# Kernel optimization log

Hardware: AMD Instinct MI355X
Metric: run time of the kernel (lower is better)

The kernel has to match this reference:

```python
import jax, jax.numpy as jnp
import numpy as np

B = 131072
IN_DIM = 21   # velocity_dim * (past_frame + 2) = 3 * 7
HID = 512
OUT_DIM = 21  # 7 waypoints * 3 coords
SEG = 0.5     # segment width in in_same_segment
WW = 0.5      # rescale weight for same-segment elements
INVALID = -10000.0
VALID_THRESH = -5000.0


def setup_inputs() -> dict:
    key = jax.random.key(0)
    ks = jax.random.split(key, 9)
    velocities = jax.random.normal(ks[0], (B, IN_DIM), dtype=jnp.float32)
    gt = jax.random.normal(ks[1], (B, 7, 3), dtype=jnp.float32)
    # emulate warp_gt padding: some trailing waypoints are invalid sentinels
    pad_mask = jax.random.bernoulli(ks[2], 0.2, (B, 7, 1))
    gt = jnp.where(pad_mask, jnp.float32(INVALID), gt)
    s1 = 1.0 / np.sqrt(IN_DIM)
    s2 = 1.0 / np.sqrt(HID)
    W1 = jax.random.uniform(ks[3], (HID, IN_DIM), jnp.float32, -s1, s1)
    b1 = jax.random.uniform(ks[4], (HID,), jnp.float32, -s1, s1)
    W2 = jax.random.uniform(ks[5], (HID, HID), jnp.float32, -s2, s2)
    b2 = jax.random.uniform(ks[6], (HID,), jnp.float32, -s2, s2)
    W3 = jax.random.uniform(ks[7], (OUT_DIM, HID), jnp.float32, -s2, s2)
    b3 = jax.random.uniform(ks[8], (OUT_DIM,), jnp.float32, -s2, s2)
    return {"velocities": velocities, "gt": gt,
            "W1": W1, "b1": b1, "W2": W2, "b2": b2, "W3": W3, "b3": b3}


def reference(velocities, gt, W1, b1, W2, b2, W3, b3):
    # plan_head MLP: 21 -> 512 -> 512 -> 21
    h = jax.nn.relu(velocities @ W1.T + b1)
    h = jax.nn.relu(h @ W2.T + b2)
    out = h @ W3.T + b3                      # [B, 21]
    pred = out.reshape(-1, 7, 3)             # waypoints x1..x7, 3 coords each
    # segment-conditional weighted L1 loss (vectorized form of the Python loop)
    valid = gt > VALID_THRESH
    same_seg = jnp.floor(pred / SEG) == jnp.floor(gt / SEG)
    w = jnp.where(valid & same_seg, jnp.float32(WW), jnp.float32(1.0))
    diff = jnp.abs(pred * w - gt * w)
    num = jnp.sum(jnp.where(valid, diff, 0.0))
    den = jnp.sum(valid.astype(jnp.float32))
    return num / den
```

## Files before the change

### kernel.cpp

```cpp
#include <hip/hip_runtime.h>
#include <hip/hip_bf16.h>

typedef __bf16 bf16_t;
typedef __bf16 bf16x4 __attribute__((ext_vector_type(4)));
typedef __bf16 bf16x8 __attribute__((ext_vector_type(8)));
typedef float f32x4 __attribute__((ext_vector_type(4)));

#define IN_DIM 21
#define HID 512
#define OUT_DIM 21
#define M_TILE 128
#define THREADS 1024

__device__ __forceinline__ int swz(int row, int col) {
    return col ^ ((row & 7) << 3);
}

__global__ void prep_kernel(const float* __restrict__ W1, const float* __restrict__ W2,
                            const float* __restrict__ W3,
                            bf16_t* __restrict__ W1f, bf16_t* __restrict__ W2f,
                            bf16_t* __restrict__ W3f, float* __restrict__ accum) {
    if (blockIdx.x == 0 && threadIdx.x == 0) {
        accum[0] = 0.0f; accum[1] = 0.0f;
        ((unsigned*)accum)[2] = 0u;
    }
    int i = blockIdx.x * blockDim.x + threadIdx.x;
    int stride = gridDim.x * blockDim.x;
    const int NW2 = HID * HID;
    const int NW1 = 32 * 512;
    const int NW3 = 16 * 2 * 512;
    for (; i < NW2 + NW1 + NW3; i += stride) {
        if (i < NW2) {
            int j = i & 7, lane = (i >> 3) & 63, ntile = (i >> 9) & 31, kstep = i >> 14;
            int n = ntile * 16 + (lane & 15);
            int k = kstep * 32 + (lane >> 4) * 8 + j;
            W2f[i] = (bf16_t)W2[n * HID + k];
        } else if (i < NW2 + NW1) {
            int t = i - NW2;
            int j = t & 7, lane = (t >> 3) & 63, ntile = t >> 9;
            int n = ntile * 16 + (lane & 15);
            int k = (lane >> 4) * 8 + j;
            W1f[t] = (k < IN_DIM) ? (bf16_t)W1[n * IN_DIM + k] : (bf16_t)0.0f;
        } else {
            int t = i - NW2 - NW1;
            int j = t & 7, lane = (t >> 3) & 63, ot = (t >> 9) & 1, kstep = t >> 10;
            int o = ot * 16 + (lane & 15);
            int k = kstep * 32 + (lane >> 4) * 8 + j;
            W3f[t] = (o < OUT_DIM) ? (bf16_t)W3[o * HID + k] : (bf16_t)0.0f;
        }
    }
}

__global__ __launch_bounds__(THREADS, 4)
void fused_kernel(const float* __restrict__ V, const float* __restrict__ gt,
                  const float* __restrict__ b1, const float* __restrict__ b2,
                  const float* __restrict__ b3,
                  const bf16_t* __restrict__ W1f, const bf16_t* __restrict__ W2f,
                  const bf16_t* __restrict__ W3f, float* __restrict__ accum,
                  float* __restrict__ out) {
    __shared__ __align__(16) bf16_t vlds[M_TILE][40];
    __shared__ __align__(16) bf16_t h[M_TILE][HID];
    __shared__ float redbuf[32];

    const int tid  = threadIdx.x;
    const int wave = tid >> 6;
    const int lane = tid & 63;
    const int quad = lane >> 4;
    const int l16  = lane & 15;
    const int mh   = wave >> 3;
    const int ng   = wave & 7;
    const int sx   = (l16 & 7) << 3;
    const long row0 = (long)blockIdx.x * M_TILE;

    const bf16_t* w2p = W2f + ng * 4 * 512 + lane * 8;
    bf16x8 awA[4], awB[4];
    #pragma unroll
    for (int nt = 0; nt < 4; ++nt)
        awA[nt] = *reinterpret_cast<const bf16x8*>(w2p + nt * 512);

    for (int idx = tid; idx < M_TILE * 32; idx += THREADS) {
        int r = idx >> 5, c = idx & 31;
        float v = (c < IN_DIM) ? V[(row0 + r) * IN_DIM + c] : 0.0f;
        vlds[r][c] = (bf16_t)v;
    }
    __syncthreads();

    {
        bf16x8 bv[4];
        #pragma unroll
        for (int mt = 0; mt < 4; ++mt)
            bv[mt] = *reinterpret_cast<const bf16x8*>(&vlds[mh * 64 + mt * 16 + l16][quad * 8]);
        #pragma unroll
        for (int nt = 0; nt < 4; ++nt) {
            int ntile = ng * 4 + nt;
            bf16x8 aw = *reinterpret_cast<const bf16x8*>(W1f + ntile * 512 + lane * 8);
            f32x4 bias = *reinterpret_cast<const f32x4*>(b1 + ntile * 16 + quad * 4);
            int n0 = ntile * 16 + quad * 4;
            #pragma unroll
            for (int mt = 0; mt < 4; ++mt) {
                f32x4 c = {0.0f, 0.0f, 0.0f, 0.0f};
                c = __builtin_amdgcn_mfma_f32_16x16x32_bf16(aw, bv[mt], c, 0, 0, 0);
                bf16x4 pk;
                #pragma unroll
                for (int r = 0; r < 4; ++r) {
                    float v = c[r] + bias[r];
                    pk[r] = (bf16_t)(v > 0.0f ? v : 0.0f);
                }
                int m = mh * 64 + mt * 16 + l16;
                *reinterpret_cast<bf16x4*>(&h[m][n0 ^ sx]) = pk;
            }
        }
    }
    __syncthreads();

    {
        f32x4 acc[4][4];
        #pragma unroll
        for (int mt = 0; mt < 4; ++mt)
            #pragma unroll
            for (int nt = 0; nt < 4; ++nt)
                acc[mt][nt] = (f32x4){0.0f, 0.0f, 0.0f, 0.0f};

        #pragma unroll 1
        for (int ks = 0; ks < 16; ks += 2) {
            #pragma unroll
            for (int nt = 0; nt < 4; ++nt)
                awB[nt] = *reinterpret_cast<const bf16x8*>(w2p + (ks + 1) * 16384 + nt * 512);
            {
                bf16x8 bh[4];
                #pragma unroll
                for (int mt = 0; mt < 4; ++mt)
                    bh[mt] = *reinterpret_cast<const bf16x8*>(
                        &h[mh * 64 + mt * 16 + l16][(ks * 32 + quad * 8) ^ sx]);
                #pragma unroll
                for (int mt = 0; mt < 4; ++mt)
                    #pragma unroll
                    for (int nt = 0; nt < 4; ++nt)
                        acc[mt][nt] = __builtin_amdgcn_mfma_f32_16x16x32_bf16(awA[nt], bh[mt], acc[mt][nt], 0, 0, 0);
            }
            #pragma unroll
            for (int nt = 0; nt < 4; ++nt)
                awA[nt] = *reinterpret_cast<const bf16x8*>(w2p + (ks + 2) * 16384 + nt * 512);
            {
                bf16x8 bh[4];
                #pragma unroll
                for (int mt = 0; mt < 4; ++mt)
                    bh[mt] = *reinterpret_cast<const bf16x8*>(
                        &h[mh * 64 + mt * 16 + l16][((ks + 1) * 32 + quad * 8) ^ sx]);
                #pragma unroll
                for (int mt = 0; mt < 4; ++mt)
                    #pragma unroll
                    for (int nt = 0; nt < 4; ++nt)
                        acc[mt][nt] = __builtin_amdgcn_mfma_f32_16x16x32_bf16(awB[nt], bh[mt], acc[mt][nt], 0, 0, 0);
            }
        }
        __syncthreads();

        #pragma unroll
        for (int nt = 0; nt < 4; ++nt) {
            int ntile = ng * 4 + nt;
            f32x4 bias = *reinterpret_cast<const f32x4*>(b2 + ntile * 16 + quad * 4);
            int n0 = ntile * 16 + quad * 4;
            #pragma unroll
            for (int mt = 0; mt < 4; ++mt) {
                bf16x4 pk;
                #pragma unroll
                for (int r = 0; r < 4; ++r) {
                    float v = acc[mt][nt][r] + bias[r];
                    pk[r] = (bf16_t)(v > 0.0f ? v : 0.0f);
                }
                int m = mh * 64 + mt * 16 + l16;
                *reinterpret_cast<bf16x4*>(&h[m][n0 ^ sx]) = pk;
            }
        }
    }
    __syncthreads();

    {
        const int mt = wave >> 1;
        const int ot = wave & 1;
        const int o0 = ot * 16 + quad * 4;
        const long grow = row0 + mt * 16 + l16;

        float g[4], b3v[4];
        #pragma unroll
        for (int r = 0; r < 4; ++r) {
            bool v = (o0 + r) < OUT_DIM;
            g[r]   = v ? gt[grow * OUT_DIM + o0 + r] : -10000.0f;
            b3v[r] = v ? b3[o0 + r] : 0.0f;
        }

        f32x4 acc3a = {0.0f, 0.0f, 0.0f, 0.0f};
        f32x4 acc3b = {0.0f, 0.0f, 0.0f, 0.0f};
        const int rr = mt * 16 + l16;
        #pragma unroll
        for (int ks = 0; ks < 16; ks += 2) {
            bf16x8 bh0 = *reinterpret_cast<const bf16x8*>(&h[rr][(ks * 32 + quad * 8) ^ sx]);
            bf16x8 bh1 = *reinterpret_cast<const bf16x8*>(&h[rr][((ks + 1) * 32 + quad * 8) ^ sx]);
            bf16x8 aw0 = *reinterpret_cast<const bf16x8*>(W3f + (ks * 2 + ot) * 512 + lane * 8);
            bf16x8 aw1 = *reinterpret_cast<const bf16x8*>(W3f + ((ks + 1) * 2 + ot) * 512 + lane * 8);
            acc3a = __builtin_amdgcn_mfma_f32_16x16x32_bf16(aw0, bh0, acc3a, 0, 0, 0);
            acc3b = __builtin_amdgcn_mfma_f32_16x16x32_bf16(aw1, bh1, acc3b, 0, 0, 0);
        }

        float num = 0.0f, den = 0.0f;
        #pragma unroll
        for (int r = 0; r < 4; ++r) {
            if ((o0 + r) < OUT_DIM) {
                float pred = acc3a[r] + acc3b[r] + b3v[r];
                if (g[r] > -5000.0f) {
                    float w = (floorf(pred * 2.0f) == floorf(g[r] * 2.0f)) ? 0.5f : 1.0f;
                    num += fabsf(pred * w - g[r] * w);
                    den += 1.0f;
                }
            }
        }
        #pragma unroll
        for (int off = 32; off > 0; off >>= 1) {
            num += __shfl_down(num, off);
            den += __shfl_down(den, off);
        }
        if (lane == 0) { redbuf[wave * 2] = num; redbuf[wave * 2 + 1] = den; }
    }
    __syncthreads();
    if (tid == 0) {
        float nB = 0.0f, dB = 0.0f;
        #pragma unroll
        for (int w = 0; w < 16; ++w) { nB += redbuf[w * 2]; dB += redbuf[w * 2 + 1]; }
        atomicAdd(accum, nB);
        atomicAdd(accum + 1, dB);
        __threadfence();
        unsigned prev = atomicAdd((unsigned*)(accum + 2), 1u);
        if (prev == gridDim.x - 1) {
            __threadfence();
            float num = __hip_atomic_load(accum,     __ATOMIC_RELAXED, __HIP_MEMORY_SCOPE_AGENT);
            float den = __hip_atomic_load(accum + 1, __ATOMIC_RELAXED, __HIP_MEMORY_SCOPE_AGENT);
            out[0] = num / den;
        }
    }
}

extern "C" void kernel_launch(void* const* d_in, const int* in_sizes, int n_in,
                              void* d_out, int out_size, void* d_ws, size_t ws_size,
                              hipStream_t stream) {
    const float* V  = (const float*)d_in[0];
    const float* gt = (const float*)d_in[1];
    const float* W1 = (const float*)d_in[2];
    const float* b1 = (const float*)d_in[3];
    const float* W2 = (const float*)d_in[4];
    const float* b2 = (const float*)d_in[5];
    const float* W3 = (const float*)d_in[6];
    const float* b3 = (const float*)d_in[7];
    float* out = (float*)d_out;

    char* ws = (char*)d_ws;
    float* accum = (float*)ws;
    bf16_t* W2f = (bf16_t*)(ws + 16);
    bf16_t* W1f = (bf16_t*)(ws + 16 + 512 * 512 * 2);
    bf16_t* W3f = (bf16_t*)(ws + 16 + 512 * 512 * 2 + 32 * 512 * 2);

    int Brows = in_sizes[0] / IN_DIM;
    int grid = Brows / M_TILE;

    prep_kernel<<<576, 512, 0, stream>>>(W1, W2, W3, W1f, W2f, W3f, accum);
    fused_kernel<<<grid, THREADS, 0, stream>>>(V, gt, b1, b2, b3, W1f, W2f, W3f, accum, out);
}
```

Baseline: 193.4 us.

## Halve row tile per block and double-buffer hidden-state fragments in layer 2

Halves the row tile to 64 and the block to 512 threads (8 waves). Each wave now covers all 64 rows for its 4 output tiles, which shrinks LDS so two blocks can share a CU and overlap each other's barrier phases. The layer-2 loop now double-buffers the LDS hidden fragments and uses a single register set of W2 fragments, reloading each right after its MFMAs are issued. Biases are folded into the MFMA accumulator initial values. The cost is that each block streams the full W2 for half as many rows, doubling W2 traffic through L2.

```diff
diff --git a/kernel.cpp b/kernel.cpp
--- a/kernel.cpp
+++ b/kernel.cpp
@@ -9,8 +9,8 @@
 #define IN_DIM 21
 #define HID 512
 #define OUT_DIM 21
-#define M_TILE 128
-#define THREADS 1024
+#define M_TILE 64
+#define THREADS 512
 
 __device__ __forceinline__ int swz(int row, int col) {
     return col ^ ((row & 7) << 3);
@@ -60,23 +60,21 @@
                   float* __restrict__ out) {
     __shared__ __align__(16) bf16_t vlds[M_TILE][40];
     __shared__ __align__(16) bf16_t h[M_TILE][HID];
-    __shared__ float redbuf[32];
+    __shared__ float redbuf[16];
 
     const int tid  = threadIdx.x;
     const int wave = tid >> 6;
     const int lane = tid & 63;
     const int quad = lane >> 4;
     const int l16  = lane & 15;
-    const int mh   = wave >> 3;
-    const int ng   = wave & 7;
     const int sx   = (l16 & 7) << 3;
     const long row0 = (long)blockIdx.x * M_TILE;
 
-    const bf16_t* w2p = W2f + ng * 4 * 512 + lane * 8;
-    bf16x8 awA[4], awB[4];
+    const bf16_t* w2p = W2f + wave * 4 * 512 + lane * 8;
+    bf16x8 aw[4];
     #pragma unroll
     for (int nt = 0; nt < 4; ++nt)
-        awA[nt] = *reinterpret_cast<const bf16x8*>(w2p + nt * 512);
+        aw[nt] = *reinterpret_cast<const bf16x8*>(w2p + nt * 512);
 
     for (int idx = tid; idx < M_TILE * 32; idx += THREADS) {
         int r = idx >> 5, c = idx & 31;
@@ -89,24 +87,22 @@
         bf16x8 bv[4];
         #pragma unroll
         for (int mt = 0; mt < 4; ++mt)
-            bv[mt] = *reinterpret_cast<const bf16x8*>(&vlds[mh * 64 + mt * 16 + l16][quad * 8]);
+            bv[mt] = *reinterpret_cast<const bf16x8*>(&vlds[mt * 16 + l16][quad * 8]);
         #pragma unroll
         for (int nt = 0; nt < 4; ++nt) {
-            int ntile = ng * 4 + nt;
-            bf16x8 aw = *reinterpret_cast<const bf16x8*>(W1f + ntile * 512 + lane * 8);
+            int ntile = wave * 4 + nt;
+            bf16x8 w1 = *reinterpret_cast<const bf16x8*>(W1f + ntile * 512 + lane * 8);
             f32x4 bias = *reinterpret_cast<const f32x4*>(b1 + ntile * 16 + quad * 4);
             int n0 = ntile * 16 + quad * 4;
             #pragma unroll
             for (int mt = 0; mt < 4; ++mt) {
-                f32x4 c = {0.0f, 0.0f, 0.0f, 0.0f};
-                c = __builtin_amdgcn_mfma_f32_16x16x32_bf16(aw, bv[mt], c, 0, 0, 0);
+                f32x4 c = bias;
+                c = __builtin_amdgcn_mfma_f32_16x16x32_bf16(w1, bv[mt], c, 0, 0, 0);
                 bf16x4 pk;
                 #pragma unroll
-                for (int r = 0; r < 4; ++r) {
-                    float v = c[r] + bias[r];
-                    pk[r] = (bf16_t)(v > 0.0f ? v : 0.0f);
-                }
-                int m = mh * 64 + mt * 16 + l16;
+                for (int r = 0; r < 4; ++r)
+                    pk[r] = (bf16_t)(c[r] > 0.0f ? c[r] : 0.0f);
+                int m = mt * 16 + l16;
                 *reinterpret_cast<bf16x4*>(&h[m][n0 ^ sx]) = pk;
             }
         }
@@ -116,60 +112,56 @@
     {
         f32x4 acc[4][4];
         #pragma unroll
+        for (int nt = 0; nt < 4; ++nt) {
+            f32x4 bias = *reinterpret_cast<const f32x4*>(b2 + (wave * 4 + nt) * 16 + quad * 4);
+            #pragma unroll
+            for (int mt = 0; mt < 4; ++mt)
+                acc[mt][nt] = bias;
+        }
+
+        bf16x8 bhA[4], bhB[4];
+        #pragma unroll
         for (int mt = 0; mt < 4; ++mt)
-            #pragma unroll
-            for (int nt = 0; nt < 4; ++nt)
-                acc[mt][nt] = (f32x4){0.0f, 0.0f, 0.0f, 0.0f};
+            bhA[mt] = *reinterpret_cast<const bf16x8*>(&h[mt * 16 + l16][(quad * 8) ^ sx]);
 
         #pragma unroll 1
         for (int ks = 0; ks < 16; ks += 2) {
             #pragma unroll
-            for (int nt = 0; nt < 4; ++nt)
-                awB[nt] = *reinterpret_cast<const bf16x8*>(w2p + (ks + 1) * 16384 + nt * 512);
-            {
-                bf16x8 bh[4];
+            for (int mt = 0; mt < 4; ++mt)
+                bhB[mt] = *reinterpret_cast<const bf16x8*>(
+                    &h[mt * 16 + l16][((ks + 1) * 32 + quad * 8) ^ sx]);
+            #pragma unroll
+            for (int nt = 0; nt < 4; ++nt) {
                 #pragma unroll
                 for (int mt = 0; mt < 4; ++mt)
-                    bh[mt] = *reinterpret_cast<const bf16x8*>(
-                        &h[mh * 64 + mt * 16 + l16][(ks * 32 + quad * 8) ^ sx]);
+                    acc[mt][nt] = __builtin_amdgcn_mfma_f32_16x16x32_bf16(aw[nt], bhA[mt], acc[mt][nt], 0, 0, 0);
+                aw[nt] = *reinterpret_cast<const bf16x8*>(w2p + (ks + 1) * 16384 + nt * 512);
+            }
+            const int ksn = (ks + 2) & 15;
+            #pragma unroll
+            for (int mt = 0; mt < 4; ++mt)
+                bhA[mt] = *reinterpret_cast<const bf16x8*>(
+                    &h[mt * 16 + l16][(ksn * 32 + quad * 8) ^ sx]);
+            #pragma unroll
+            for (int nt = 0; nt < 4; ++nt) {
                 #pragma unroll
                 for (int mt = 0; mt < 4; ++mt)
-                    #pragma unroll
-                    for (int nt = 0; nt < 4; ++nt)
-                        acc[mt][nt] = __builtin_amdgcn_mfma_f32_16x16x32_bf16(awA[nt], bh[mt], acc[mt][nt], 0, 0, 0);
-            }
-            #pragma unroll
-            for (int nt = 0; nt < 4; ++nt)
-                awA[nt] = *reinterpret_cast<const bf16x8*>(w2p + (ks + 2) * 16384 + nt * 512);
-            {
-                bf16x8 bh[4];
-                #pragma unroll
-                for (int mt = 0; mt < 4; ++mt)
-                    bh[mt] = *reinterpret_cast<const bf16x8*>(
-                        &h[mh * 64 + mt * 16 + l16][((ks + 1) * 32 + quad * 8) ^ sx]);
-                #pragma unroll
-                for (int mt = 0; mt < 4; ++mt)
-                    #pragma unroll
-                    for (int nt = 0; nt < 4; ++nt)
-                        acc[mt][nt] = __builtin_amdgcn_mfma_f32_16x16x32_bf16(awB[nt], bh[mt], acc[mt][nt], 0, 0, 0);
+                    acc[mt][nt] = __builtin_amdgcn_mfma_f32_16x16x32_bf16(aw[nt], bhB[mt], acc[mt][nt], 0, 0, 0);
+                aw[nt] = *reinterpret_cast<const bf16x8*>(w2p + ksn * 16384 + nt * 512);
             }
         }
         __syncthreads();
 
         #pragma unroll
         for (int nt = 0; nt < 4; ++nt) {
-            int ntile = ng * 4 + nt;
-            f32x4 bias = *reinterpret_cast<const f32x4*>(b2 + ntile * 16 + quad * 4);
-            int n0 = ntile * 16 + quad * 4;
+            int n0 = (wave * 4 + nt) * 16 + quad * 4;
             #pragma unroll
             for (int mt = 0; mt < 4; ++mt) {
                 bf16x4 pk;
                 #pragma unroll
-                for (int r = 0; r < 4; ++r) {
-                    float v = acc[mt][nt][r] + bias[r];
-                    pk[r] = (bf16_t)(v > 0.0f ? v : 0.0f);
-                }
-                int m = mh * 64 + mt * 16 + l16;
+                for (int r = 0; r < 4; ++r)
+                    pk[r] = (bf16_t)(acc[mt][nt][r] > 0.0f ? acc[mt][nt][r] : 0.0f);
+                int m = mt * 16 + l16;
                 *reinterpret_cast<bf16x4*>(&h[m][n0 ^ sx]) = pk;
             }
         }
@@ -190,7 +182,7 @@
             b3v[r] = v ? b3[o0 + r] : 0.0f;
         }
 
-        f32x4 acc3a = {0.0f, 0.0f, 0.0f, 0.0f};
+        f32x4 acc3a = {b3v[0], b3v[1], b3v[2], b3v[3]};
         f32x4 acc3b = {0.0f, 0.0f, 0.0f, 0.0f};
         const int rr = mt * 16 + l16;
         #pragma unroll
@@ -207,7 +199,7 @@
         #pragma unroll
         for (int r = 0; r < 4; ++r) {
             if ((o0 + r) < OUT_DIM) {
-                float pred = acc3a[r] + acc3b[r] + b3v[r];
+                float pred = acc3a[r] + acc3b[r];
                 if (g[r] > -5000.0f) {
                     float w = (floorf(pred * 2.0f) == floorf(g[r] * 2.0f)) ? 0.5f : 1.0f;
                     num += fabsf(pred * w - g[r] * w);
@@ -226,7 +218,7 @@
     if (tid == 0) {
         float nB = 0.0f, dB = 0.0f;
         #pragma unroll
-        for (int w = 0; w < 16; ++w) { nB += redbuf[w * 2]; dB += redbuf[w * 2 + 1]; }
+        for (int w = 0; w < 8; ++w) { nB += redbuf[w * 2]; dB += redbuf[w * 2 + 1]; }
         atomicAdd(accum, nB);
         atomicAdd(accum + 1, dB);
         __threadfence();
```

Result: slower. 293.3 us (+51.6%).
